# Kernel optimization log

Hardware: AMD Instinct MI355X
Metric: run time of the kernel (lower is better)

The kernel has to match this reference:

```python
import jax, jax.numpy as jnp
import numpy as np

B, C, H, W = 32, 128, 56, 56
O = 256
KH, KW = 3, 3
SH, SW = 1, 1
PH, PW = 1, 1
T = 6          # num_terms
R = 8          # low_rank
D = C * KH * KW          # 1152
R2 = R * KH * KW         # 72


def setup_inputs() -> dict:
    key = jax.random.key(0)
    ks = jax.random.split(key, 6)
    scale = 0.05
    return {
        "x": jax.random.normal(ks[0], (B, C, H, W), dtype=jnp.float32),
        "S1s": jax.random.normal(ks[1], (T, D, R), dtype=jnp.float32) * scale,
        "U1s": jax.random.normal(ks[2], (T, R, O), dtype=jnp.float32) * scale,
        "U2s": jax.random.normal(ks[3], (T, R2, D), dtype=jnp.float32) * scale,
        "S2s": jax.random.normal(ks[4], (T, R2, O), dtype=jnp.float32) * scale,
        "bias": jax.random.normal(ks[5], (O,), dtype=jnp.float32) * scale,
    }


def _extract_windows(x):
    # im2col: pad then gather strided windows; d flattened in (C, kh, kw) order
    xp = jnp.pad(x, ((0, 0), (0, 0), (PH, PH), (PW, PW)))
    Hp, Wp = xp.shape[2], xp.shape[3]
    Ho = (Hp - KH) // SH + 1
    Wo = (Wp - KW) // SW + 1
    # stack KH*KW shifted views -> [B, C, KH*KW, Ho, Wo]
    patches = jnp.stack(
        [xp[:, :, i:i + SH * Ho:SH, j:j + SW * Wo:SW]
         for i in range(KH) for j in range(KW)],
        axis=2,
    )
    # -> [B, Ho, Wo, C, KH*KW] -> [N, C*KH*KW]
    xw = patches.transpose(0, 3, 4, 1, 2).reshape(B * Ho * Wo, D)
    return xw, Ho, Wo


def reference(x, S1s, U1s, U2s, S2s, bias):
    xw, Ho, Wo = _extract_windows(x)                    # [N, D]
    # term 1: x_windows @ S1s[t] @ U1s[t], averaged over terms
    out1 = jnp.einsum('nd,tdr,tro->no', xw, S1s, U1s, optimize=True) / T + bias
    # term 2: x_windows @ U2s[t].T @ S2s[t], averaged over terms
    out2 = jnp.einsum('nd,tdr,tro->no', xw, jnp.swapaxes(U2s, 1, 2), S2s,
                      optimize=True) / T
    # NOTE: bias is added twice, faithfully matching the original module
    out = (out1 + out2 + bias).reshape(B, Ho, Wo, O).transpose(0, 3, 1, 2)
    return out
```

## Files before the change

### kernel.cpp

```cpp
#include <hip/hip_runtime.h>
#include <hip/hip_bf16.h>

typedef __attribute__((ext_vector_type(8))) short  short8;
typedef __attribute__((ext_vector_type(8))) unsigned short ushort8;
typedef __attribute__((ext_vector_type(4))) unsigned short usv4;
typedef __attribute__((ext_vector_type(4))) float  f32x4;

#define D_DIM 1152
#define O_DIM 256
#define N_TOT 100352
#define XT_H 58
#define XT_ROW (58 * 128)

__device__ __forceinline__ unsigned short f2bf(float f) {
  __hip_bfloat16 h = __float2bfloat16(f);
  return __builtin_bit_cast(unsigned short, h);
}

#define GLOAD_LDS16(g, l)                                              \
  __builtin_amdgcn_global_load_lds(                                    \
      (const __attribute__((address_space(1))) void*)(g),              \
      (__attribute__((address_space(3))) void*)(l), 16, 0, 0)

__global__ __launch_bounds__(256) void wt_kernel(
    const float* __restrict__ S1s, const float* __restrict__ U1s,
    const float* __restrict__ U2s, const float* __restrict__ S2s,
    unsigned short* __restrict__ Wt) {
  __shared__ float A_lds[32][64];
  __shared__ float B_lds[32][64];

  const int bo = blockIdx.x & 3;
  const int bd = blockIdx.x >> 2;
  const int o0  = bo << 6;
  const int dn0 = bd << 6;
  const int rr  = dn0 >> 7;
  const int c0  = dn0 & 127;

  const int tid = threadIdx.x;
  const int ty = tid >> 4, tx = tid & 15;

  float acc[4][4] = {};

  for (int kc = 0; kc < 15; ++kc) {
#pragma unroll
    for (int e = 0; e < 8; ++e) {
      const int li = e * 256 + tid;
      const int kk = li >> 6;
      const int xx = li & 63;
      const int k  = kc * 32 + kk;
      float av, bv;
      if (k < 48) {
        av = U1s[k * O_DIM + o0 + xx];
        const int d_old = (c0 + xx) * 9 + rr;
        bv = S1s[(size_t)((k >> 3) * D_DIM + d_old) * 8 + (k & 7)];
      } else {
        const int kq = k - 48;
        av = S2s[(size_t)kq * O_DIM + o0 + xx];
        const int d_old = (c0 + xx) * 9 + rr;
        bv = U2s[(size_t)kq * D_DIM + d_old];
      }
      A_lds[kk][xx] = av;
      B_lds[kk][xx] = bv;
    }
    __syncthreads();
#pragma unroll
    for (int kk = 0; kk < 32; ++kk) {
      f32x4 a = *(const f32x4*)&A_lds[kk][ty << 2];
      f32x4 b = *(const f32x4*)&B_lds[kk][tx << 2];
#pragma unroll
      for (int i = 0; i < 4; ++i)
#pragma unroll
        for (int j = 0; j < 4; ++j)
          acc[i][j] += a[i] * b[j];
    }
    __syncthreads();
  }

#pragma unroll
  for (int i = 0; i < 4; ++i) {
    usv4 v;
#pragma unroll
    for (int j = 0; j < 4; ++j) v[j] = f2bf(acc[i][j] * (1.0f / 6.0f));
    *(usv4*)(Wt + (size_t)(o0 + (ty << 2) + i) * D_DIM + dn0 + (tx << 2)) = v;
  }
}

__global__ __launch_bounds__(256) void pad_kernel(const float* __restrict__ x,
                                                  unsigned short* __restrict__ xt) {
  int blk = blockIdx.x;
  int b = blk / XT_H, ih = blk - b * XT_H;
  unsigned short* dst = xt + (size_t)blk * XT_ROW;
  int tid = threadIdx.x;

  if (ih == 0 || ih == XT_H - 1) {
    ushort8 z;
#pragma unroll
    for (int q = 0; q < 8; ++q) z[q] = 0;
    for (int i = tid; i < XT_ROW / 8; i += 256) ((ushort8*)dst)[i] = z;
    return;
  }

  __shared__ unsigned short lds[128 * 58];
  int h = ih - 1;
  const float* xb = x + (size_t)b * 128 * 3136 + (size_t)h * 56;
#pragma unroll 4
  for (int r = 0; r < 28; ++r) {
    int idx = r * 256 + tid;
    int c = idx / 56, w2 = idx - c * 56;
    lds[c * 58 + w2] = f2bf(xb[(size_t)c * 3136 + w2]);
  }
  __syncthreads();
#pragma unroll 4
  for (int r = 0; r < 29; ++r) {
    int idx = r * 256 + tid;
    int iw = idx >> 7, c = idx & 127;
    unsigned short v = 0;
    if (iw >= 1 && iw <= 56) v = lds[c * 58 + (iw - 1)];
    dst[idx] = v;
  }
}

__device__ __forceinline__ constexpr int KB_OFF(int kt) {
  int rr = kt >> 1;
  return ((rr / 3) * 58 + (rr % 3)) * 128 + (kt & 1) * 64;
}

#define ST_A(kts, sl2, r) \
  GLOAD_LDS16(pA[r] + (kts) * 64, smem + (sl2) * 24576 + (r) * 4096 + (w << 9))
#define ST_B(kts, sl2, r) \
  GLOAD_LDS16(pB[r] + KB_OFF(kts), smem + (sl2) * 24576 + 8192 + (r) * 4096 + (w << 9))

#define LDS_FRAG(base, row, ks)                                            \
  (*(const short8*)((const char*)(base) + (row) * 128 +                    \
     (((((ks) << 2) + (lane >> 4)) ^ ((row) & 7)) << 4)))

__global__ __launch_bounds__(512, 2) void gemm_kernel(
    const unsigned short* __restrict__ Wt, const unsigned short* __restrict__ xt,
    const float* __restrict__ bias, float* __restrict__ out) {
  __shared__ __align__(1024) unsigned short smem[3 * 24576];

  const int bid   = blockIdx.x;
  const int lid   = (bid & 7) * 98 + (bid >> 3);
  const int ntile = lid >> 1, otile = lid & 1;
  const int n0 = ntile << 8;
  const int o0 = otile << 7;

  const int tid  = threadIdx.x;
  const int w    = tid >> 6;
  const int lane = tid & 63;
  const int wm   = w >> 2;
  const int wn   = w & 3;

  const unsigned short* pA[2];
  const unsigned short* pB[4];
#pragma unroll
  for (int r = 0; r < 2; ++r) {
    const int li  = r * 512 + tid;
    const int row = li >> 3;
    const int gs  = (li & 7) ^ (row & 7);
    pA[r] = Wt + (size_t)(o0 + row) * D_DIM + gs * 8;
  }
#pragma unroll
  for (int r = 0; r < 4; ++r) {
    const int li  = r * 512 + tid;
    const int row = li >> 3;
    const int gs  = (li & 7) ^ (row & 7);
    const int n_g = n0 + row;
    const int b   = n_g / 3136;
    const int s   = n_g - b * 3136;
    const int oh  = s / 56, ow = s - oh * 56;
    pB[r] = xt + (((size_t)b * XT_H + oh) * XT_H + ow) * 128 + gs * 8;
  }

  f32x4 acc[4][4] = {};

  ST_A(0, 0, 0); ST_A(0, 0, 1);
  ST_B(0, 0, 0); ST_B(0, 0, 1); ST_B(0, 0, 2); ST_B(0, 0, 3);
  ST_A(1, 1, 0); ST_A(1, 1, 1);
  ST_B(1, 1, 0); ST_B(1, 1, 1); ST_B(1, 1, 2); ST_B(1, 1, 3);
  asm volatile("s_waitcnt vmcnt(6)" ::: "memory");
  __builtin_amdgcn_s_barrier();

#pragma unroll
  for (int kt = 0; kt < 18; ++kt) {
    const int sl  = kt % 3;
    const int kts = kt + 2;
    const int sl2 = kts % 3;
    const unsigned short* As = smem + sl * 24576;
    const unsigned short* Bs = smem + sl * 24576 + 8192;

    short8 af[4][2], bf[4][2];
#pragma unroll
    for (int mi = 0; mi < 4; ++mi) {
      const int row = (wm << 6) + (mi << 4) + (lane & 15);
      af[mi][0] = LDS_FRAG(As, row, 0);
      af[mi][1] = LDS_FRAG(As, row, 1);
    }
#pragma unroll
    for (int ni = 0; ni < 4; ++ni) {
      const int row = (wn << 6) + (ni << 4) + (lane & 15);
      bf[ni][0] = LDS_FRAG(Bs, row, 0);
      bf[ni][1] = LDS_FRAG(Bs, row, 1);
    }
    if (kts < 18) {
      ST_A(kts, sl2, 0); ST_A(kts, sl2, 1);
      ST_B(kts, sl2, 0); ST_B(kts, sl2, 1); ST_B(kts, sl2, 2); ST_B(kts, sl2, 3);
    }
    __builtin_amdgcn_s_setprio(1);
#pragma unroll
    for (int ks = 0; ks < 2; ++ks)
#pragma unroll
      for (int mi = 0; mi < 4; ++mi)
#pragma unroll
        for (int ni = 0; ni < 4; ++ni)
          acc[mi][ni] = __builtin_amdgcn_mfma_f32_16x16x32_bf16(
              af[mi][ks], bf[ni][ks], acc[mi][ni], 0, 0, 0);
    __builtin_amdgcn_s_setprio(0);
    if (kt < 16) asm volatile("s_waitcnt vmcnt(6)" ::: "memory");
    else         asm volatile("s_waitcnt vmcnt(0)" ::: "memory");
    __builtin_amdgcn_s_barrier();
  }

  const int lr = (lane >> 4) << 2;
  const int lc = lane & 15;
#pragma unroll
  for (int ni = 0; ni < 4; ++ni) {
    const int ng = n0 + (wn << 6) + (ni << 4) + lc;
    const int b  = ng / 3136;
    const int s  = ng - b * 3136;
    float* op = out + (size_t)b * (O_DIM * 3136) + s;
#pragma unroll
    for (int mi = 0; mi < 4; ++mi) {
      const int og = o0 + (wm << 6) + (mi << 4) + lr;
#pragma unroll
      for (int r = 0; r < 4; ++r)
        op[(size_t)(og + r) * 3136] = acc[mi][ni][r] + 2.0f * bias[og + r];
    }
  }
}

extern "C" void kernel_launch(void* const* d_in, const int* in_sizes, int n_in,
                              void* d_out, int out_size, void* d_ws, size_t ws_size,
                              hipStream_t stream) {
  const float* x    = (const float*)d_in[0];
  const float* S1s  = (const float*)d_in[1];
  const float* U1s  = (const float*)d_in[2];
  const float* U2s  = (const float*)d_in[3];
  const float* S2s  = (const float*)d_in[4];
  const float* bias = (const float*)d_in[5];
  float* out = (float*)d_out;
  (void)ws_size;

  unsigned short* xt = (unsigned short*)d_ws;
  unsigned short* Wt = (unsigned short*)((char*)d_ws + (size_t)32 * XT_H * XT_ROW * 2);

  pad_kernel<<<dim3(32 * XT_H), dim3(256), 0, stream>>>(x, xt);
  wt_kernel<<<dim3(72), dim3(256), 0, stream>>>(S1s, U1s, U2s, S2s, Wt);
  gemm_kernel<<<dim3(784), dim3(512), 0, stream>>>(Wt, xt, bias, out);
}
```

Baseline: 126.4 us.

## Widen GEMM tile to full output dim with split-K-half double-buffered pipeline

Each GEMM block now covers all 256 output channels for its 256 spatial positions, so every im2col activation tile is loaded once instead of twice, and the grid is halved. The k-step is split into two 32-wide halves, each with its own buffer, using a two-buffer scheme with finer-grained staging and barriers. This doubles accumulator registers per wave (8x4 MFMA tiles) and uses 128 KB of LDS. That risks occupancy and leaves 392 blocks, which may balance poorly across CUs.

```diff
diff --git a/kernel.cpp b/kernel.cpp
--- a/kernel.cpp
+++ b/kernel.cpp
@@ -120,30 +120,33 @@
   }
 }
 
-__device__ __forceinline__ constexpr int KB_OFF(int kt) {
+#define ABYTE(bf_, ks_) ((bf_) * 65536 + (ks_) * 16384)
+#define BBYTE(bf_, ks_) ((bf_) * 65536 + 32768 + (ks_) * 16384)
+
+__device__ __forceinline__ constexpr int KOF(int kt) {
   int rr = kt >> 1;
   return ((rr / 3) * 58 + (rr % 3)) * 128 + (kt & 1) * 64;
 }
 
-#define ST_A(kts, sl2, r) \
-  GLOAD_LDS16(pA[r] + (kts) * 64, smem + (sl2) * 24576 + (r) * 4096 + (w << 9))
-#define ST_B(kts, sl2, r) \
-  GLOAD_LDS16(pB[r] + KB_OFF(kts), smem + (sl2) * 24576 + 8192 + (r) * 4096 + (w << 9))
-
-#define LDS_FRAG(base, row, ks)                                            \
-  (*(const short8*)((const char*)(base) + (row) * 128 +                    \
-     (((((ks) << 2) + (lane >> 4)) ^ ((row) & 7)) << 4)))
+#define STAGE(kt_, ks_, bf_) do {                                              \
+  GLOAD_LDS16(pA0 + (kt_) * 64 + (ks_) * 32,                                   \
+              smem + (ABYTE(bf_, ks_) >> 1) + stoff0);                         \
+  GLOAD_LDS16(pA1 + (kt_) * 64 + (ks_) * 32,                                   \
+              smem + (ABYTE(bf_, ks_) >> 1) + stoff1);                         \
+  GLOAD_LDS16(pB0 + KOF(kt_) + (ks_) * 32,                                     \
+              smem + (BBYTE(bf_, ks_) >> 1) + stoff0);                         \
+  GLOAD_LDS16(pB1 + KOF(kt_) + (ks_) * 32,                                     \
+              smem + (BBYTE(bf_, ks_) >> 1) + stoff1);                         \
+} while (0)
 
 __global__ __launch_bounds__(512, 2) void gemm_kernel(
     const unsigned short* __restrict__ Wt, const unsigned short* __restrict__ xt,
     const float* __restrict__ bias, float* __restrict__ out) {
-  __shared__ __align__(1024) unsigned short smem[3 * 24576];
+  __shared__ __align__(1024) unsigned short smem[65536];
 
   const int bid   = blockIdx.x;
-  const int lid   = (bid & 7) * 98 + (bid >> 3);
-  const int ntile = lid >> 1, otile = lid & 1;
-  const int n0 = ntile << 8;
-  const int o0 = otile << 7;
+  const int ntile = (bid & 7) * 49 + (bid >> 3);
+  const int n0    = ntile << 8;
 
   const int tid  = threadIdx.x;
   const int w    = tid >> 6;
@@ -151,87 +154,89 @@
   const int wm   = w >> 2;
   const int wn   = w & 3;
 
-  const unsigned short* pA[2];
-  const unsigned short* pB[4];
-#pragma unroll
-  for (int r = 0; r < 2; ++r) {
-    const int li  = r * 512 + tid;
-    const int row = li >> 3;
-    const int gs  = (li & 7) ^ (row & 7);
-    pA[r] = Wt + (size_t)(o0 + row) * D_DIM + gs * 8;
-  }
-#pragma unroll
-  for (int r = 0; r < 4; ++r) {
-    const int li  = r * 512 + tid;
-    const int row = li >> 3;
-    const int gs  = (li & 7) ^ (row & 7);
-    const int n_g = n0 + row;
-    const int b   = n_g / 3136;
-    const int s   = n_g - b * 3136;
-    const int oh  = s / 56, ow = s - oh * 56;
-    pB[r] = xt + (((size_t)b * XT_H + oh) * XT_H + ow) * 128 + gs * 8;
-  }
-
-  f32x4 acc[4][4] = {};
-
-  ST_A(0, 0, 0); ST_A(0, 0, 1);
-  ST_B(0, 0, 0); ST_B(0, 0, 1); ST_B(0, 0, 2); ST_B(0, 0, 3);
-  ST_A(1, 1, 0); ST_A(1, 1, 1);
-  ST_B(1, 1, 0); ST_B(1, 1, 1); ST_B(1, 1, 2); ST_B(1, 1, 3);
-  asm volatile("s_waitcnt vmcnt(6)" ::: "memory");
+  const int stoff0 = w << 9;
+  const int stoff1 = 4096 + (w << 9);
+
+  const unsigned short *pA0, *pA1, *pB0, *pB1;
+  {
+    const int li0 = tid, li1 = 512 + tid;
+    const int r0 = li0 >> 2, g0 = (li0 & 3) ^ (r0 & 3);
+    const int r1 = li1 >> 2, g1 = (li1 & 3) ^ (r1 & 3);
+    pA0 = Wt + (size_t)r0 * D_DIM + g0 * 8;
+    pA1 = Wt + (size_t)r1 * D_DIM + g1 * 8;
+    int n_g0 = n0 + r0;
+    int b0 = n_g0 / 3136, s0 = n_g0 - b0 * 3136;
+    int oh0 = s0 / 56, ow0 = s0 - oh0 * 56;
+    pB0 = xt + (((size_t)b0 * XT_H + oh0) * XT_H + ow0) * 128 + g0 * 8;
+    int n_g1 = n0 + r1;
+    int b1 = n_g1 / 3136, s1 = n_g1 - b1 * 3136;
+    int oh1 = s1 / 56, ow1 = s1 - oh1 * 56;
+    pB1 = xt + (((size_t)b1 * XT_H + oh1) * XT_H + ow1) * 128 + g1 * 8;
+  }
+
+  f32x4 acc[8][4] = {};
+
+  const int la15 = lane & 15;
+  const int frq  = (((lane >> 4) ^ (lane & 3)) << 4);
+
+  STAGE(0, 0, 0);
+  STAGE(0, 1, 0);
+  STAGE(1, 0, 1);
+  asm volatile("s_waitcnt vmcnt(8)" ::: "memory");
   __builtin_amdgcn_s_barrier();
 
 #pragma unroll
   for (int kt = 0; kt < 18; ++kt) {
-    const int sl  = kt % 3;
-    const int kts = kt + 2;
-    const int sl2 = kts % 3;
-    const unsigned short* As = smem + sl * 24576;
-    const unsigned short* Bs = smem + sl * 24576 + 8192;
-
-    short8 af[4][2], bf[4][2];
-#pragma unroll
-    for (int mi = 0; mi < 4; ++mi) {
-      const int row = (wm << 6) + (mi << 4) + (lane & 15);
-      af[mi][0] = LDS_FRAG(As, row, 0);
-      af[mi][1] = LDS_FRAG(As, row, 1);
-    }
-#pragma unroll
-    for (int ni = 0; ni < 4; ++ni) {
-      const int row = (wn << 6) + (ni << 4) + (lane & 15);
-      bf[ni][0] = LDS_FRAG(Bs, row, 0);
-      bf[ni][1] = LDS_FRAG(Bs, row, 1);
-    }
-    if (kts < 18) {
-      ST_A(kts, sl2, 0); ST_A(kts, sl2, 1);
-      ST_B(kts, sl2, 0); ST_B(kts, sl2, 1); ST_B(kts, sl2, 2); ST_B(kts, sl2, 3);
-    }
-    __builtin_amdgcn_s_setprio(1);
-#pragma unroll
-    for (int ks = 0; ks < 2; ++ks)
-#pragma unroll
-      for (int mi = 0; mi < 4; ++mi)
+    const int bsel = kt & 1;
+#pragma unroll
+    for (int p = 0; p < 2; ++p) {
+      const char* Abase = (const char*)smem + ABYTE(bsel, p);
+      const char* Bbase = (const char*)smem + BBYTE(bsel, p);
+
+      short8 af[8], bfr[4];
+#pragma unroll
+      for (int mi = 0; mi < 8; ++mi)
+        af[mi] = *(const short8*)(Abase + ((wm << 7) + (mi << 4) + la15) * 64 + frq);
+#pragma unroll
+      for (int ni = 0; ni < 4; ++ni)
+        bfr[ni] = *(const short8*)(Bbase + ((wn << 6) + (ni << 4) + la15) * 64 + frq);
+
+      if (p == 0) {
+        if (kt + 1 < 18) STAGE(kt + 1, 1, (kt + 1) & 1);
+      } else {
+        if (kt + 2 < 18) STAGE(kt + 2, 0, kt & 1);
+      }
+      __builtin_amdgcn_s_barrier();
+
+      __builtin_amdgcn_s_setprio(1);
+#pragma unroll
+      for (int mi = 0; mi < 8; ++mi)
 #pragma unroll
         for (int ni = 0; ni < 4; ++ni)
           acc[mi][ni] = __builtin_amdgcn_mfma_f32_16x16x32_bf16(
-              af[mi][ks], bf[ni][ks], acc[mi][ni], 0, 0, 0);
-    __builtin_amdgcn_s_setprio(0);
-    if (kt < 16) asm volatile("s_waitcnt vmcnt(6)" ::: "memory");
-    else         asm volatile("s_waitcnt vmcnt(0)" ::: "memory");
-    __builtin_amdgcn_s_barrier();
+              af[mi], bfr[ni], acc[mi][ni], 0, 0, 0);
+      __builtin_amdgcn_s_setprio(0);
+
+      if (kt < 16 || (kt == 16 && p == 0))
+        asm volatile("s_waitcnt vmcnt(8)" ::: "memory");
+      else if (kt == 16)
+        asm volatile("s_waitcnt vmcnt(4)" ::: "memory");
+      else if (kt == 17 && p == 0)
+        asm volatile("s_waitcnt vmcnt(0)" ::: "memory");
+      __builtin_amdgcn_s_barrier();
+    }
   }
 
   const int lr = (lane >> 4) << 2;
-  const int lc = lane & 15;
 #pragma unroll
   for (int ni = 0; ni < 4; ++ni) {
-    const int ng = n0 + (wn << 6) + (ni << 4) + lc;
+    const int ng = n0 + (wn << 6) + (ni << 4) + la15;
     const int b  = ng / 3136;
     const int s  = ng - b * 3136;
     float* op = out + (size_t)b * (O_DIM * 3136) + s;
 #pragma unroll
-    for (int mi = 0; mi < 4; ++mi) {
-      const int og = o0 + (wm << 6) + (mi << 4) + lr;
+    for (int mi = 0; mi < 8; ++mi) {
+      const int og = (wm << 7) + (mi << 4) + lr;
 #pragma unroll
       for (int r = 0; r < 4; ++r)
         op[(size_t)(og + r) * 3136] = acc[mi][ni][r] + 2.0f * bias[og + r];
@@ -256,5 +261,5 @@
 
   pad_kernel<<<dim3(32 * XT_H), dim3(256), 0, stream>>>(x, xt);
   wt_kernel<<<dim3(72), dim3(256), 0, stream>>>(S1s, U1s, U2s, S2s, Wt);
-  gemm_kernel<<<dim3(784), dim3(512), 0, stream>>>(Wt, xt, bias, out);
-}
+  gemm_kernel<<<dim3(392), dim3(512), 0, stream>>>(Wt, xt, bias, out);
+}
```

Result: slower. 134.4 us (+6.4%).
